# Performance work log

Hardware: AMD Instinct MI355X
Metric: run time of the kernel (lower is better)

Reference implementation:

```python
import jax, jax.numpy as jnp
import numpy as np

B, M = 512, 2048            # batch of src-tgt pairs, sampled walk positions per pair
NUM_KEYS = 1_000_000        # unique (node, time) keys in nodetime2emb map
NUM_NODES = 100_000
LP = 4                      # num_layers + 1 (saw encoding width)
ENC = 32                    # enc_dim
FEAT = 64                   # node feature dim (MergeLayer dim2)
D3, D4 = 64, 1              # MergeLayer hidden / output dims


def setup_inputs() -> dict:
    key = jax.random.key(0)
    ks = jax.random.split(key, 12)
    s = 0.05
    return {
        "pos_table": jax.random.uniform(ks[0], (NUM_KEYS, LP), dtype=jnp.float32),
        "node_feat": jax.random.normal(ks[1], (NUM_NODES, FEAT), dtype=jnp.float32),
        "W1": jax.random.normal(ks[2], (LP, ENC), dtype=jnp.float32) * s,
        "b1": jnp.zeros((ENC,), dtype=jnp.float32),
        "W2": jax.random.normal(ks[3], (ENC, ENC), dtype=jnp.float32) * s,
        "b2": jnp.zeros((ENC,), dtype=jnp.float32),
        "Wm1": jax.random.normal(ks[4], (ENC + FEAT, D3), dtype=jnp.float32) * s,
        "bm1": jnp.zeros((D3,), dtype=jnp.float32),
        "Wm2": jax.random.normal(ks[5], (D3, D4), dtype=jnp.float32) * s,
        "bm2": jnp.zeros((D4,), dtype=jnp.float32),
        "key_idx": jax.random.randint(ks[6], (B, M), 0, NUM_KEYS, dtype=jnp.int32),
        "node_idx": jax.random.randint(ks[7], (B, M), 0, NUM_NODES, dtype=jnp.int32),
    }


def reference(pos_table, node_feat, W1, b1, W2, b2, Wm1, bm1, Wm2, bm2, key_idx, node_idx):
    # PositionEncoder.forward: gather saw encodings by (node, time) key,
    # then trainable_embedding = Linear(LP->ENC) -> ReLU -> Linear(ENC->ENC)
    enc = pos_table[key_idx]                       # [B, M, LP] irregular gather
    pe = jax.nn.relu(enc @ W1 + b1) @ W2 + b2      # [B, M, ENC]
    # gather raw node features for the same walk positions
    feat = node_feat[node_idx]                     # [B, M, FEAT] irregular gather
    # MergeLayer (non_linear=True): concat -> fc1 -> ReLU -> fc2
    x = jnp.concatenate([pe, feat], axis=-1)       # [B, M, ENC+FEAT]
    z = jax.nn.relu(x @ Wm1 + bm1) @ Wm2 + bm2     # [B, M, 1]
    return z
```

## Files before the change

### kernel.cpp

```cpp
#include <hip/hip_runtime.h>


typedef _Float16 half8 __attribute__((ext_vector_type(8)));
typedef float floatx4 __attribute__((ext_vector_type(4)));

#define HSTR 40
#define WSTR 104
#define GRID 768

__global__ void feat_to_f16(const float* __restrict__ nf,
                            _Float16* __restrict__ o, int n8) {
    int t = blockIdx.x * 256 + threadIdx.x;
    if (t >= n8) return;
    const float4* p = (const float4*)nf + (size_t)t * 2;
    const float4 a = p[0], b = p[1];
    half8 h;
    h[0] = (_Float16)a.x; h[1] = (_Float16)a.y;
    h[2] = (_Float16)a.z; h[3] = (_Float16)a.w;
    h[4] = (_Float16)b.x; h[5] = (_Float16)b.y;
    h[6] = (_Float16)b.z; h[7] = (_Float16)b.w;
    *((half8*)o + t) = h;
}

__global__ __launch_bounds__(256, 3) void neurtw_mfma(
    const float* __restrict__ pos_table,
    const float* __restrict__ node_feat,
    const float* __restrict__ W1,
    const float* __restrict__ b1,
    const float* __restrict__ W2,
    const float* __restrict__ b2,
    const float* __restrict__ Wm1,
    const float* __restrict__ bm1,
    const float* __restrict__ Wm2,
    const float* __restrict__ bm2,
    const int*   __restrict__ key_idx,
    const int*   __restrict__ node_idx,
    const _Float16* __restrict__ feat16,
    int use_f16,
    float*       __restrict__ out,
    int rows)
{
    __shared__ _Float16 hpe[256 * HSTR];
    __shared__ _Float16 wm1t[64 * WSTR];

    const int tid  = threadIdx.x;
    const int lane = tid & 63;
    const int r0   = (tid >> 6) * 64;
    const int ln   = lane & 15;
    const int q    = lane >> 4;

    #pragma unroll
    for (int i = 0; i < 3; ++i) {
        const int task = i * 256 + tid;
        const int n = task & 63, k8 = task >> 6;
        half8 w;
        #pragma unroll
        for (int kk = 0; kk < 8; ++kk)
            w[kk] = (_Float16)Wm1[(k8 * 8 + kk) * 64 + n];
        *(half8*)(&wm1t[n * WSTR + k8 * 8]) = w;
    }

    half8 b_w2[2];
    #pragma unroll
    for (int ct = 0; ct < 2; ++ct)
        #pragma unroll
        for (int j = 0; j < 8; ++j)
            b_w2[ct][j] = (_Float16)W2[(q * 8 + j) * 32 + ct * 16 + ln];
    float b2v[2];
    b2v[0] = b2[ln]; b2v[1] = b2[16 + ln];
    float bm1v[4], wm2v[4];
    #pragma unroll
    for (int ct = 0; ct < 4; ++ct) {
        bm1v[ct] = bm1[ct * 16 + ln];
        wm2v[ct] = Wm2[ct * 16 + ln];
    }
    const float bm2s = bm2[0];

    __syncthreads();

    for (int base = blockIdx.x * 256; base < rows; base += GRID * 256) {
        const int row = base + tid;

        int ndr[4];
        #pragma unroll
        for (int rt = 0; rt < 4; ++rt)
            ndr[rt] = node_idx[base + r0 + rt * 16 + ln];

        half8 fA[4][2];
        if (use_f16) {
            #pragma unroll
            for (int rt = 0; rt < 4; ++rt) {
                const _Float16* fb = feat16 + (size_t)ndr[rt] * 64 + q * 8;
                fA[rt][0] = *(const half8*)(fb);
                fA[rt][1] = *(const half8*)(fb + 32);
            }
        } else {
            #pragma unroll
            for (int rt = 0; rt < 4; ++rt) {
                const float* fb = node_feat + (size_t)ndr[rt] * 64 + q * 8;
                #pragma unroll
                for (int kt = 0; kt < 2; ++kt) {
                    const float4 lo = *(const float4*)(fb + kt * 32);
                    const float4 hi = *(const float4*)(fb + kt * 32 + 4);
                    half8 h;
                    h[0] = (_Float16)lo.x; h[1] = (_Float16)lo.y;
                    h[2] = (_Float16)lo.z; h[3] = (_Float16)lo.w;
                    h[4] = (_Float16)hi.x; h[5] = (_Float16)hi.y;
                    h[6] = (_Float16)hi.z; h[7] = (_Float16)hi.w;
                    fA[rt][kt] = h;
                }
            }
        }

        const int kk = key_idx[row];
        const float4 enc = *(const float4*)(pos_table + (size_t)kk * 4);

        #pragma unroll
        for (int g = 0; g < 4; ++g) {
            half8 hv;
            #pragma unroll
            for (int j8 = 0; j8 < 8; ++j8) {
                const int j = g * 8 + j8;
                float a = fmaf(enc.w, W1[96 + j],
                          fmaf(enc.z, W1[64 + j],
                          fmaf(enc.y, W1[32 + j],
                          fmaf(enc.x, W1[j], b1[j]))));
                hv[j8] = (_Float16)fmaxf(a, 0.0f);
            }
            *(half8*)(&hpe[tid * HSTR + g * 8]) = hv;
        }
        __syncthreads();

        half8 a_h[4];
        #pragma unroll
        for (int rt = 0; rt < 4; ++rt)
            a_h[rt] = *(const half8*)(&hpe[(r0 + rt * 16 + ln) * HSTR + q * 8]);

        floatx4 pc[4][2];
        #pragma unroll
        for (int rt = 0; rt < 4; ++rt)
            #pragma unroll
            for (int ct = 0; ct < 2; ++ct) {
                floatx4 c = {0.f, 0.f, 0.f, 0.f};
                pc[rt][ct] = __builtin_amdgcn_mfma_f32_16x16x32_f16(
                    a_h[rt], b_w2[ct], c, 0, 0, 0);
            }

        #pragma unroll
        for (int rt = 0; rt < 4; ++rt)
            #pragma unroll
            for (int ct = 0; ct < 2; ++ct)
                #pragma unroll
                for (int r = 0; r < 4; ++r)
                    hpe[(r0 + rt * 16 + q * 4 + r) * HSTR + ct * 16 + ln] =
                        (_Float16)(pc[rt][ct][r] + b2v[ct]);
        __syncthreads();

        floatx4 acc[4][4];
        #pragma unroll
        for (int ct = 0; ct < 4; ++ct) {
            const float bb = bm1v[ct];
            #pragma unroll
            for (int rt = 0; rt < 4; ++rt)
                acc[rt][ct] = (floatx4){bb, bb, bb, bb};
        }

        {
            half8 a_pe[4];
            #pragma unroll
            for (int rt = 0; rt < 4; ++rt)
                a_pe[rt] = *(const half8*)(&hpe[(r0 + rt * 16 + ln) * HSTR + q * 8]);
            half8 b0[4];
            #pragma unroll
            for (int ct = 0; ct < 4; ++ct)
                b0[ct] = *(const half8*)(&wm1t[(ct * 16 + ln) * WSTR + q * 8]);
            #pragma unroll
            for (int rt = 0; rt < 4; ++rt)
                #pragma unroll
                for (int ct = 0; ct < 4; ++ct)
                    acc[rt][ct] = __builtin_amdgcn_mfma_f32_16x16x32_f16(
                        a_pe[rt], b0[ct], acc[rt][ct], 0, 0, 0);
        }

        #pragma unroll
        for (int kt = 0; kt < 2; ++kt) {
            half8 bk[4];
            #pragma unroll
            for (int ct = 0; ct < 4; ++ct)
                bk[ct] = *(const half8*)(&wm1t[(ct * 16 + ln) * WSTR + 32 + kt * 32 + q * 8]);
            #pragma unroll
            for (int rt = 0; rt < 4; ++rt)
                #pragma unroll
                for (int ct = 0; ct < 4; ++ct)
                    acc[rt][ct] = __builtin_amdgcn_mfma_f32_16x16x32_f16(
                        fA[rt][kt], bk[ct], acc[rt][ct], 0, 0, 0);
        }

        #pragma unroll
        for (int rt = 0; rt < 4; ++rt) {
            #pragma unroll
            for (int r = 0; r < 4; ++r) {
                float p = 0.0f;
                #pragma unroll
                for (int ct = 0; ct < 4; ++ct)
                    p = fmaf(fmaxf(acc[rt][ct][r], 0.0f), wm2v[ct], p);
                p += __shfl_xor(p, 1);
                p += __shfl_xor(p, 2);
                p += __shfl_xor(p, 4);
                p += __shfl_xor(p, 8);
                if (ln == 0)
                    out[base + r0 + rt * 16 + q * 4 + r] = p + bm2s;
            }
        }
    }
}

extern "C" void kernel_launch(void* const* d_in, const int* in_sizes, int n_in,
                              void* d_out, int out_size, void* d_ws, size_t ws_size,
                              hipStream_t stream) {
    const float* pos_table = (const float*)d_in[0];
    const float* node_feat = (const float*)d_in[1];
    const float* W1        = (const float*)d_in[2];
    const float* b1        = (const float*)d_in[3];
    const float* W2        = (const float*)d_in[4];
    const float* b2        = (const float*)d_in[5];
    const float* Wm1       = (const float*)d_in[6];
    const float* bm1       = (const float*)d_in[7];
    const float* Wm2       = (const float*)d_in[8];
    const float* bm2       = (const float*)d_in[9];
    const int*   key_idx   = (const int*)d_in[10];
    const int*   node_idx  = (const int*)d_in[11];
    float* out = (float*)d_out;

    const int rows = in_sizes[10];
    const int nfeat = in_sizes[1];
    const size_t need = (size_t)nfeat * sizeof(_Float16);
    const int use_f16 = (ws_size >= need) ? 1 : 0;

    if (use_f16) {
        const int n8 = nfeat / 8;
        feat_to_f16<<<(n8 + 255) / 256, 256, 0, stream>>>(
            node_feat, (_Float16*)d_ws, n8);
    }

    neurtw_mfma<<<GRID, 256, 0, stream>>>(
        pos_table, node_feat, W1, b1, W2, b2, Wm1, bm1, Wm2, bm2,
        key_idx, node_idx, (const _Float16*)d_ws, use_f16, out, rows);
}
```

Before: 158.9 us.

## Fold W2 into Wm1 to drop the second positional-encoding GEMM

Because there is no nonlinearity between Linear(ENC->ENC) and the first MergeLayer layer, a small extra kernel precomputes W2·Wm1[:32] and the fused bias b2·Wm1[:32]+bm1. The main kernel then multiplies the ReLU hidden directly by the fused matrix. This removes one MFMA stage, an LDS write-back and two block barriers per tile. The grid is also raised from 768 to 1024 blocks. It adds a tiny one-block launch, and the fp16 rounding of the fused weights changes numerics slightly.

```diff
diff --git a/kernel.cpp b/kernel.cpp
--- a/kernel.cpp
+++ b/kernel.cpp
@@ -6,7 +6,7 @@
 
 #define HSTR 40
 #define WSTR 104
-#define GRID 768
+#define GRID_MAIN 1024
 
 __global__ void feat_to_f16(const float* __restrict__ nf,
                             _Float16* __restrict__ o, int n8) {
@@ -22,26 +22,50 @@
     *((half8*)o + t) = h;
 }
 
-__global__ __launch_bounds__(256, 3) void neurtw_mfma(
+__global__ void make_wfuse(const float* __restrict__ W2,
+                           const float* __restrict__ Wm1,
+                           const float* __restrict__ b2,
+                           const float* __restrict__ bm1,
+                           float* __restrict__ wfuse,
+                           float* __restrict__ bfuse) {
+    const int t = threadIdx.x;
+    #pragma unroll
+    for (int u = 0; u < 8; ++u) {
+        const int e = t * 8 + u, i = e >> 6, c = e & 63;
+        float s = 0.f;
+        #pragma unroll
+        for (int n = 0; n < 32; ++n)
+            s = fmaf(W2[i * 32 + n], Wm1[n * 64 + c], s);
+        wfuse[i * 64 + c] = s;
+    }
+    if (t < 64) {
+        float s = bm1[t];
+        #pragma unroll
+        for (int n = 0; n < 32; ++n)
+            s = fmaf(b2[n], Wm1[n * 64 + t], s);
+        bfuse[t] = s;
+    }
+}
+
+__global__ __launch_bounds__(256, 3) void neurtw_r6(
     const float* __restrict__ pos_table,
     const float* __restrict__ node_feat,
     const float* __restrict__ W1,
     const float* __restrict__ b1,
-    const float* __restrict__ W2,
-    const float* __restrict__ b2,
     const float* __restrict__ Wm1,
-    const float* __restrict__ bm1,
     const float* __restrict__ Wm2,
     const float* __restrict__ bm2,
     const int*   __restrict__ key_idx,
     const int*   __restrict__ node_idx,
+    const float* __restrict__ wfuse,
+    const float* __restrict__ bfuse,
     const _Float16* __restrict__ feat16,
     int use_f16,
     float*       __restrict__ out,
     int rows)
 {
-    __shared__ _Float16 hpe[256 * HSTR];
-    __shared__ _Float16 wm1t[64 * WSTR];
+    __shared__ _Float16 hbuf[256 * HSTR];
+    __shared__ _Float16 bmat[64 * WSTR];
 
     const int tid  = threadIdx.x;
     const int lane = tid & 63;
@@ -53,32 +77,25 @@
     for (int i = 0; i < 3; ++i) {
         const int task = i * 256 + tid;
         const int n = task & 63, k8 = task >> 6;
+        const float* src = (k8 < 4) ? wfuse : Wm1;
         half8 w;
         #pragma unroll
         for (int kk = 0; kk < 8; ++kk)
-            w[kk] = (_Float16)Wm1[(k8 * 8 + kk) * 64 + n];
-        *(half8*)(&wm1t[n * WSTR + k8 * 8]) = w;
-    }
-
-    half8 b_w2[2];
-    #pragma unroll
-    for (int ct = 0; ct < 2; ++ct)
-        #pragma unroll
-        for (int j = 0; j < 8; ++j)
-            b_w2[ct][j] = (_Float16)W2[(q * 8 + j) * 32 + ct * 16 + ln];
-    float b2v[2];
-    b2v[0] = b2[ln]; b2v[1] = b2[16 + ln];
-    float bm1v[4], wm2v[4];
+            w[kk] = (_Float16)src[(k8 * 8 + kk) * 64 + n];
+        *(half8*)(&bmat[n * WSTR + k8 * 8]) = w;
+    }
+
+    float bfusev[4], wm2v[4];
     #pragma unroll
     for (int ct = 0; ct < 4; ++ct) {
-        bm1v[ct] = bm1[ct * 16 + ln];
-        wm2v[ct] = Wm2[ct * 16 + ln];
+        bfusev[ct] = bfuse[ct * 16 + ln];
+        wm2v[ct]   = Wm2[ct * 16 + ln];
     }
     const float bm2s = bm2[0];
 
     __syncthreads();
 
-    for (int base = blockIdx.x * 256; base < rows; base += GRID * 256) {
+    for (int base = blockIdx.x * 256; base < rows; base += GRID_MAIN * 256) {
         const int row = base + tid;
 
         int ndr[4];
@@ -127,59 +144,33 @@
                           fmaf(enc.x, W1[j], b1[j]))));
                 hv[j8] = (_Float16)fmaxf(a, 0.0f);
             }
-            *(half8*)(&hpe[tid * HSTR + g * 8]) = hv;
-        }
-        __syncthreads();
-
+            *(half8*)(&hbuf[tid * HSTR + g * 8]) = hv;
+        }
         half8 a_h[4];
         #pragma unroll
         for (int rt = 0; rt < 4; ++rt)
-            a_h[rt] = *(const half8*)(&hpe[(r0 + rt * 16 + ln) * HSTR + q * 8]);
-
-        floatx4 pc[4][2];
-        #pragma unroll
-        for (int rt = 0; rt < 4; ++rt)
-            #pragma unroll
-            for (int ct = 0; ct < 2; ++ct) {
-                floatx4 c = {0.f, 0.f, 0.f, 0.f};
-                pc[rt][ct] = __builtin_amdgcn_mfma_f32_16x16x32_f16(
-                    a_h[rt], b_w2[ct], c, 0, 0, 0);
-            }
-
-        #pragma unroll
-        for (int rt = 0; rt < 4; ++rt)
-            #pragma unroll
-            for (int ct = 0; ct < 2; ++ct)
-                #pragma unroll
-                for (int r = 0; r < 4; ++r)
-                    hpe[(r0 + rt * 16 + q * 4 + r) * HSTR + ct * 16 + ln] =
-                        (_Float16)(pc[rt][ct][r] + b2v[ct]);
-        __syncthreads();
+            a_h[rt] = *(const half8*)(&hbuf[(r0 + rt * 16 + ln) * HSTR + q * 8]);
 
         floatx4 acc[4][4];
         #pragma unroll
         for (int ct = 0; ct < 4; ++ct) {
-            const float bb = bm1v[ct];
+            const float bb = bfusev[ct];
             #pragma unroll
             for (int rt = 0; rt < 4; ++rt)
                 acc[rt][ct] = (floatx4){bb, bb, bb, bb};
         }
 
         {
-            half8 a_pe[4];
-            #pragma unroll
-            for (int rt = 0; rt < 4; ++rt)
-                a_pe[rt] = *(const half8*)(&hpe[(r0 + rt * 16 + ln) * HSTR + q * 8]);
             half8 b0[4];
             #pragma unroll
             for (int ct = 0; ct < 4; ++ct)
-                b0[ct] = *(const half8*)(&wm1t[(ct * 16 + ln) * WSTR + q * 8]);
+                b0[ct] = *(const half8*)(&bmat[(ct * 16 + ln) * WSTR + q * 8]);
             #pragma unroll
             for (int rt = 0; rt < 4; ++rt)
                 #pragma unroll
                 for (int ct = 0; ct < 4; ++ct)
                     acc[rt][ct] = __builtin_amdgcn_mfma_f32_16x16x32_f16(
-                        a_pe[rt], b0[ct], acc[rt][ct], 0, 0, 0);
+                        a_h[rt], b0[ct], acc[rt][ct], 0, 0, 0);
         }
 
         #pragma unroll
@@ -187,7 +178,7 @@
             half8 bk[4];
             #pragma unroll
             for (int ct = 0; ct < 4; ++ct)
-                bk[ct] = *(const half8*)(&wm1t[(ct * 16 + ln) * WSTR + 32 + kt * 32 + q * 8]);
+                bk[ct] = *(const half8*)(&bmat[(ct * 16 + ln) * WSTR + 32 + kt * 32 + q * 8]);
             #pragma unroll
             for (int rt = 0; rt < 4; ++rt)
                 #pragma unroll
@@ -232,18 +223,22 @@
     const int*   node_idx  = (const int*)d_in[11];
     float* out = (float*)d_out;
 
-    const int rows = in_sizes[10];
+    const int rows  = in_sizes[10];
     const int nfeat = in_sizes[1];
-    const size_t need = (size_t)nfeat * sizeof(_Float16);
-    const int use_f16 = (ws_size >= need) ? 1 : 0;
+
+    float*    wfuse  = (float*)d_ws;
+    float*    bfuse  = (float*)((char*)d_ws + 8192);
+    _Float16* feat16 = (_Float16*)((char*)d_ws + 16384);
+    const size_t need_f16 = 16384 + (size_t)nfeat * sizeof(_Float16);
+    const int use_f16 = (ws_size >= need_f16) ? 1 : 0;
 
     if (use_f16) {
         const int n8 = nfeat / 8;
-        feat_to_f16<<<(n8 + 255) / 256, 256, 0, stream>>>(
-            node_feat, (_Float16*)d_ws, n8);
-    }
-
-    neurtw_mfma<<<GRID, 256, 0, stream>>>(
-        pos_table, node_feat, W1, b1, W2, b2, Wm1, bm1, Wm2, bm2,
-        key_idx, node_idx, (const _Float16*)d_ws, use_f16, out, rows);
-}
+        feat_to_f16<<<(n8 + 255) / 256, 256, 0, stream>>>(node_feat, feat16, n8);
+    }
+    make_wfuse<<<1, 256, 0, stream>>>(W2, Wm1, b2, bm1, wfuse, bfuse);
+
+    neurtw_r6<<<GRID_MAIN, 256, 0, stream>>>(
+        pos_table, node_feat, W1, b1, Wm1, Wm2, bm2,
+        key_idx, node_idx, wfuse, bfuse, feat16, use_f16, out, rows);
+}
```

Measured after the change: 195.7 us. 1.23x slower.
